# Kernel optimization log

Measured on AMD Instinct MI355X. Metric: run time of the kernel, lower is better.

The kernel has to match this reference:

```python
import jax, jax.numpy as jnp
import numpy as np

N_NODES = 50000
N_EDGES = 800000
D = 128
NEG_SLOPE = 0.01
LN_EPS = 1e-5


def gcn_conv(x, W, b, src, dst, n_nodes):
    # Linear transform: [N, D_in] @ [D_in, D_out]
    h = x @ W
    # Symmetric degree normalization (self-loops already included in src/dst)
    deg = jax.ops.segment_sum(jnp.ones_like(dst, dtype=h.dtype), dst, num_segments=n_nodes)
    dinv = jnp.where(deg > 0, jax.lax.rsqrt(deg), 0.0)
    coef = dinv[src] * dinv[dst]                      # [E]
    msg = h[src] * coef[:, None]                      # gather + scale, [E, D]
    out = jax.ops.segment_sum(msg, dst, num_segments=n_nodes)  # scatter-add
    return out + b


def layer_norm(x, gamma, beta):
    mu = jnp.mean(x, axis=-1, keepdims=True)
    var = jnp.mean(jnp.square(x - mu), axis=-1, keepdims=True)
    return (x - mu) * jax.lax.rsqrt(var + LN_EPS) * gamma + beta


def setup_inputs() -> dict:
    key = jax.random.key(0)
    ks = jax.random.split(key, 8)
    x = jax.random.normal(ks[0], (N_NODES, D), dtype=jnp.float32)
    edge_index = jax.random.randint(ks[1], (2, N_EDGES), 0, N_NODES, dtype=jnp.int64)
    s = 1.0 / np.sqrt(D)
    W1 = jax.random.uniform(ks[2], (D, D), jnp.float32, -s, s)
    b1 = jnp.zeros((D,), jnp.float32)
    W2 = jax.random.uniform(ks[3], (D, D), jnp.float32, -s, s)
    b2 = jnp.zeros((D,), jnp.float32)
    ln1_g = jnp.ones((D,), jnp.float32)
    ln1_b = jnp.zeros((D,), jnp.float32)
    ln2_g = jnp.ones((D,), jnp.float32)
    ln2_b = jnp.zeros((D,), jnp.float32)
    return {"x": x, "edge_index": edge_index, "W1": W1, "b1": b1,
            "ln1_g": ln1_g, "ln1_b": ln1_b, "W2": W2, "b2": b2,
            "ln2_g": ln2_g, "ln2_b": ln2_b}


def reference(x, edge_index, W1, b1, ln1_g, ln1_b, W2, b2, ln2_g, ln2_b):
    n = x.shape[0]
    # add self-loops (PyG GCNConv default)
    loops = jnp.arange(n, dtype=edge_index.dtype)
    src = jnp.concatenate([edge_index[0], loops])
    dst = jnp.concatenate([edge_index[1], loops])

    residual = x
    h = gcn_conv(x, W1, b1, src, dst, n)
    h = jax.nn.leaky_relu(h, NEG_SLOPE)
    h = layer_norm(h + residual, ln1_g, ln1_b)
    h = gcn_conv(h, W2, b2, src, dst, n)
    return jax.nn.leaky_relu(layer_norm(h + residual, ln2_g, ln2_b), NEG_SLOPE)
```

## Files before the change

### kernel.cpp

```cpp
#include <hip/hip_runtime.h>
#include <hip/hip_bf16.h>

#define NN 50000
#define NE 800000
#define D 128
#define NEG_SLOPE 0.01f
#define LN_EPS 1e-5f

#define NPB 256
#define NB 196
#define CAP 6144
#define ECH 8192
#define NCH ((NE + ECH - 1) / ECH)

typedef __attribute__((ext_vector_type(8))) short bf16x8;
typedef __attribute__((ext_vector_type(4))) float f32x4;

__device__ inline unsigned short f2bf(float f) {
    unsigned u = __float_as_uint(f);
    unsigned r = 0x7FFFu + ((u >> 16) & 1u);
    return (unsigned short)((u + r) >> 16);
}
__device__ inline void bf2x(unsigned u, float& lo, float& hi) {
    lo = __uint_as_float(u << 16);
    hi = __uint_as_float(u & 0xFFFF0000u);
}


__global__ __launch_bounds__(256) void bucket_scatter(const int* __restrict__ src,
                                                      const int* __restrict__ dst,
                                                      int* __restrict__ bcursor,
                                                      int2* __restrict__ bedge, int ne) {
    __shared__ int2 stage[ECH];
    __shared__ int hist[NB], lofs[NB], lcur[NB], gbase[NB];
    __shared__ int tmp[256];
    int t = threadIdx.x;
    int e0 = blockIdx.x * ECH;
    int ecnt = min(ECH, ne - e0);
    if (t < NB) hist[t] = 0;
    __syncthreads();
    for (int k = t; k < ecnt; k += 256) atomicAdd(&hist[dst[e0 + k] >> 8], 1);
    __syncthreads();
    int v = (t < NB) ? hist[t] : 0;
    tmp[t] = v;
    __syncthreads();
    for (int off = 1; off < 256; off <<= 1) {
        int u = (t >= off) ? tmp[t - off] : 0;
        __syncthreads();
        tmp[t] += u;
        __syncthreads();
    }
    if (t < NB) {
        lofs[t] = tmp[t] - v;
        lcur[t] = tmp[t] - v;
        gbase[t] = atomicAdd(&bcursor[t], v);
    }
    __syncthreads();
    for (int k = t; k < ecnt; k += 256) {
        int s = src[e0 + k], d = dst[e0 + k];
        int p = atomicAdd(&lcur[d >> 8], 1);
        stage[p] = make_int2(s, d);
    }
    __syncthreads();
    for (int k = t; k < ecnt; k += 256) {
        int2 eg = stage[k];
        int b = eg.y >> 8;
        bedge[(size_t)b * CAP + gbase[b] + (k - lofs[b])] = eg;
    }
}

__global__ __launch_bounds__(256) void node_count(const int2* __restrict__ bedge,
                                                  const int* __restrict__ bcnt,
                                                  float* __restrict__ dinv,
                                                  int* __restrict__ prowtmp,
                                                  int* __restrict__ pbsum) {
    __shared__ int h[NPB];
    __shared__ int tmp[256];
    int b = blockIdx.x, t = threadIdx.x;
    h[t] = 0;
    __syncthreads();
    int s0 = b * CAP, s1 = s0 + bcnt[b];
    for (int k = s0 + t; k < s1; k += 256) atomicAdd(&h[bedge[k].y & 255], 1);
    __syncthreads();
    int deg = h[t];
    int node = b * NPB + t;
    if (node < NN) dinv[node] = rsqrtf((float)(deg + 1));
    int pdeg = (deg + 7) & ~7;
    tmp[t] = pdeg;
    __syncthreads();
    for (int off = 1; off < 256; off <<= 1) {
        int u = (t >= off) ? tmp[t - off] : 0;
        __syncthreads();
        tmp[t] += u;
        __syncthreads();
    }
    prowtmp[b * NPB + t] = tmp[t] - pdeg;
    if (t == 255) pbsum[b] = tmp[255];
}

__global__ void pbucket_scan(const int* __restrict__ pbsum, int* __restrict__ pbstart,
                             int* __restrict__ rowstart_nn) {
    __shared__ int tmp[256];
    int t = threadIdx.x;
    int v = (t < NB) ? pbsum[t] : 0;
    tmp[t] = v;
    __syncthreads();
    for (int off = 1; off < 256; off <<= 1) {
        int u = (t >= off) ? tmp[t - off] : 0;
        __syncthreads();
        tmp[t] += u;
        __syncthreads();
    }
    if (t < NB) pbstart[t] = tmp[t] - v;
    if (t == 255) *rowstart_nn = tmp[255];
}

__global__ __launch_bounds__(256) void csr_scatter(const int2* __restrict__ bedge,
                                                   const int* __restrict__ bcnt,
                                                   const int* __restrict__ pbstart,
                                                   const int* __restrict__ prowtmp,
                                                   const float* __restrict__ dinv,
                                                   int* __restrict__ rowstart,
                                                   int2* __restrict__ csr_pair) {
    __shared__ int cur[NPB];
    __shared__ int rl[NPB];
    int b = blockIdx.x, t = threadIdx.x;
    int base = pbstart[b];
    int node = b * NPB + t;
    int r = base + prowtmp[node];
    rl[t] = r;
    cur[t] = 0;
    if (node < NN) rowstart[node] = r;
    __syncthreads();
    int s0 = b * CAP, s1 = s0 + bcnt[b];
    for (int k = s0 + t; k < s1; k += 256) {
        int2 eg = bedge[k];
        int li = eg.y & 255;
        int p = atomicAdd(&cur[li], 1);
        float coef = dinv[eg.x] * dinv[eg.y];
        csr_pair[rl[li] + p] = make_int2(eg.x, __float_as_int(coef));
    }
    __syncthreads();
    int deg = cur[t];
    int pend = (deg + 7) & ~7;
    int selfsrc = (node < NN) ? node : 0;
    for (int k = deg; k < pend; ++k)
        csr_pair[rl[t] + k] = make_int2(selfsrc, 0);
}

__global__ void wt_pack2(const float* __restrict__ W1, const float* __restrict__ W2,
                         unsigned short* __restrict__ WT1, unsigned short* __restrict__ WT2) {
    int tid = blockIdx.x * 256 + threadIdx.x;
    const float* W = (tid < D * D) ? W1 : W2;
    unsigned short* WT = (tid < D * D) ? WT1 : WT2;
    int id = tid & (D * D - 1);
    int nn = id & 127, k = id >> 7;
    WT[nn * 128 + k] = f2bf(W[k * 128 + nn]);
}

__global__ __launch_bounds__(256) void gemm_mfma(const float* __restrict__ A,
                                                 const unsigned short* __restrict__ WT,
                                                 unsigned short* __restrict__ out, int n) {
    __shared__ __align__(16) unsigned short a_lds[64 * 128];
    __shared__ __align__(16) unsigned short w_lds[128 * 128];
    int t = threadIdx.x;
    int m0 = blockIdx.x * 64;

    #pragma unroll
    for (int it = 0; it < 8; ++it) {
        int idx = it * 256 + t;
        int row = idx >> 4, c = idx & 15;
        uint4 v = *(const uint4*)&WT[row * 128 + c * 8];
        int byte = (row * 256 + c * 16) ^ ((row & 7) << 4);
        *(uint4*)((char*)w_lds + byte) = v;
    }
    #pragma unroll
    for (int it = 0; it < 4; ++it) {
        int idx = it * 256 + t;
        int row = idx >> 4, c = idx & 15;
        int grow = m0 + row;
        float4 v0 = make_float4(0.f, 0.f, 0.f, 0.f), v1 = v0;
        if (grow < n) {
            v0 = *(const float4*)&A[(size_t)grow * D + c * 8];
            v1 = *(const float4*)&A[(size_t)grow * D + c * 8 + 4];
        }
        uint2 lo, hi;
        lo.x = (unsigned)f2bf(v0.x) | ((unsigned)f2bf(v0.y) << 16);
        lo.y = (unsigned)f2bf(v0.z) | ((unsigned)f2bf(v0.w) << 16);
        hi.x = (unsigned)f2bf(v1.x) | ((unsigned)f2bf(v1.y) << 16);
        hi.y = (unsigned)f2bf(v1.z) | ((unsigned)f2bf(v1.w) << 16);
        int byte = (row * 256 + c * 16) ^ ((row & 7) << 4);
        *(uint4*)((char*)a_lds + byte) = make_uint4(lo.x, lo.y, hi.x, hi.y);
    }
    __syncthreads();

    int wv = t >> 6, l = t & 63;
    int lrow = l & 15, lgrp = l >> 4;
    int arow = wv * 16 + lrow;

    f32x4 acc[8];
    #pragma unroll
    for (int nf = 0; nf < 8; ++nf) acc[nf] = (f32x4){0.f, 0.f, 0.f, 0.f};

    #pragma unroll
    for (int kk = 0; kk < 4; ++kk) {
        int abyte = (arow * 256 + kk * 64 + lgrp * 16) ^ ((arow & 7) << 4);
        bf16x8 afrag = *(bf16x8*)((char*)a_lds + abyte);
        #pragma unroll
        for (int nf = 0; nf < 8; ++nf) {
            int bcol = nf * 16 + lrow;
            int bbyte = (bcol * 256 + kk * 64 + lgrp * 16) ^ ((bcol & 7) << 4);
            bf16x8 bfrag = *(bf16x8*)((char*)w_lds + bbyte);
            acc[nf] = __builtin_amdgcn_mfma_f32_16x16x32_bf16(afrag, bfrag, acc[nf], 0, 0, 0);
        }
    }

    #pragma unroll
    for (int nf = 0; nf < 8; ++nf) {
        #pragma unroll
        for (int r = 0; r < 4; ++r) {
            int grow = m0 + wv * 16 + lgrp * 4 + r;
            if (grow < n) {
                int col = nf * 16 + lrow;
                out[(size_t)grow * D + col] = f2bf(acc[nf][r]);
            }
        }
    }
}


__device__ inline void agg8(const unsigned* __restrict__ h, const int2* __restrict__ csr_pair,
                            int e, int lane, float& accx, float& accy) {
    int4 q0 = *(const int4*)&csr_pair[e + 0];
    int4 q1 = *(const int4*)&csr_pair[e + 2];
    int4 q2 = *(const int4*)&csr_pair[e + 4];
    int4 q3 = *(const int4*)&csr_pair[e + 6];
    unsigned g0 = h[(size_t)q0.x * (D / 2) + lane];
    unsigned g1 = h[(size_t)q0.z * (D / 2) + lane];
    unsigned g2 = h[(size_t)q1.x * (D / 2) + lane];
    unsigned g3 = h[(size_t)q1.z * (D / 2) + lane];
    unsigned g4 = h[(size_t)q2.x * (D / 2) + lane];
    unsigned g5 = h[(size_t)q2.z * (D / 2) + lane];
    unsigned g6 = h[(size_t)q3.x * (D / 2) + lane];
    unsigned g7 = h[(size_t)q3.z * (D / 2) + lane];
    float ax, ay, c;
    c = __int_as_float(q0.y); bf2x(g0, ax, ay); accx = fmaf(c, ax, accx); accy = fmaf(c, ay, accy);
    c = __int_as_float(q0.w); bf2x(g1, ax, ay); accx = fmaf(c, ax, accx); accy = fmaf(c, ay, accy);
    c = __int_as_float(q1.y); bf2x(g2, ax, ay); accx = fmaf(c, ax, accx); accy = fmaf(c, ay, accy);
    c = __int_as_float(q1.w); bf2x(g3, ax, ay); accx = fmaf(c, ax, accx); accy = fmaf(c, ay, accy);
    c = __int_as_float(q2.y); bf2x(g4, ax, ay); accx = fmaf(c, ax, accx); accy = fmaf(c, ay, accy);
    c = __int_as_float(q2.w); bf2x(g5, ax, ay); accx = fmaf(c, ax, accx); accy = fmaf(c, ay, accy);
    c = __int_as_float(q3.y); bf2x(g6, ax, ay); accx = fmaf(c, ax, accx); accy = fmaf(c, ay, accy);
    c = __int_as_float(q3.w); bf2x(g7, ax, ay); accx = fmaf(c, ax, accx); accy = fmaf(c, ay, accy);
}

template <int MODE>
__device__ inline float2 ln_norm(float v0, float v1, float2 gv, float2 bt) {
    float s1 = v0 + v1, s2 = v0 * v0 + v1 * v1;
    #pragma unroll
    for (int off = 1; off < 64; off <<= 1) {
        s1 += __shfl_xor(s1, off, 64);
        s2 += __shfl_xor(s2, off, 64);
    }
    float mu = s1 * (1.f / 128.f);
    float var = fmaxf(s2 * (1.f / 128.f) - mu * mu, 0.f);
    float rs = rsqrtf(var + LN_EPS);
    float o0 = (v0 - mu) * rs * gv.x + bt.x;
    float o1 = (v1 - mu) * rs * gv.y + bt.y;
    if (MODE == 1) {
        o0 = o0 > 0.f ? o0 : NEG_SLOPE * o0;
        o1 = o1 > 0.f ? o1 : NEG_SLOPE * o1;
    }
    return make_float2(o0, o1);
}

template <int MODE>
__global__ __launch_bounds__(256) void agg_ln(const unsigned* __restrict__ h,
                                              const float* __restrict__ x,
                                              const float* __restrict__ bias,
                                              const float* __restrict__ gamma,
                                              const float* __restrict__ beta,
                                              const float* __restrict__ dinv,
                                              const int* __restrict__ rowstart,
                                              const int2* __restrict__ csr_pair,
                                              float* __restrict__ out) {
    int wid = threadIdx.x >> 6;
    int lane = threadIdx.x & 63;
    int iA = blockIdx.x * 8 + wid * 2;
    int iB = iA + 1;
    float diA = dinv[iA], diB = dinv[iB];
    size_t rowA = (size_t)iA * D + 2 * lane;
    size_t rowB = (size_t)iB * D + 2 * lane;

    float hx, hy;
    bf2x(h[(size_t)iA * (D / 2) + lane], hx, hy);
    float aAx = diA * diA * hx, aAy = diA * diA * hy;
    bf2x(h[(size_t)iB * (D / 2) + lane], hx, hy);
    float aBx = diB * diB * hx, aBy = diB * diB * hy;

    int eA = __builtin_amdgcn_readfirstlane(rowstart[iA]);
    int eA1 = __builtin_amdgcn_readfirstlane(rowstart[iA + 1]);
    int eB = __builtin_amdgcn_readfirstlane(rowstart[iB]);
    int eB1 = __builtin_amdgcn_readfirstlane(rowstart[iB + 1]);

    while (eA < eA1 && eB < eB1) {
        int4 qA0 = *(const int4*)&csr_pair[eA + 0];
        int4 qA1 = *(const int4*)&csr_pair[eA + 2];
        int4 qA2 = *(const int4*)&csr_pair[eA + 4];
        int4 qA3 = *(const int4*)&csr_pair[eA + 6];
        int4 qB0 = *(const int4*)&csr_pair[eB + 0];
        int4 qB1 = *(const int4*)&csr_pair[eB + 2];
        int4 qB2 = *(const int4*)&csr_pair[eB + 4];
        int4 qB3 = *(const int4*)&csr_pair[eB + 6];
        unsigned gA0 = h[(size_t)qA0.x * (D / 2) + lane];
        unsigned gA1 = h[(size_t)qA0.z * (D / 2) + lane];
        unsigned gA2 = h[(size_t)qA1.x * (D / 2) + lane];
        unsigned gA3 = h[(size_t)qA1.z * (D / 2) + lane];
        unsigned gA4 = h[(size_t)qA2.x * (D / 2) + lane];
        unsigned gA5 = h[(size_t)qA2.z * (D / 2) + lane];
        unsigned gA6 = h[(size_t)qA3.x * (D / 2) + lane];
        unsigned gA7 = h[(size_t)qA3.z * (D / 2) + lane];
        unsigned gB0 = h[(size_t)qB0.x * (D / 2) + lane];
        unsigned gB1 = h[(size_t)qB0.z * (D / 2) + lane];
        unsigned gB2 = h[(size_t)qB1.x * (D / 2) + lane];
        unsigned gB3 = h[(size_t)qB1.z * (D / 2) + lane];
        unsigned gB4 = h[(size_t)qB2.x * (D / 2) + lane];
        unsigned gB5 = h[(size_t)qB2.z * (D / 2) + lane];
        unsigned gB6 = h[(size_t)qB3.x * (D / 2) + lane];
        unsigned gB7 = h[(size_t)qB3.z * (D / 2) + lane];
        float ax, ay, c;
        c = __int_as_float(qA0.y); bf2x(gA0, ax, ay); aAx = fmaf(c, ax, aAx); aAy = fmaf(c, ay, aAy);
        c = __int_as_float(qA0.w); bf2x(gA1, ax, ay); aAx = fmaf(c, ax, aAx); aAy = fmaf(c, ay, aAy);
        c = __int_as_float(qA1.y); bf2x(gA2, ax, ay); aAx = fmaf(c, ax, aAx); aAy = fmaf(c, ay, aAy);
        c = __int_as_float(qA1.w); bf2x(gA3, ax, ay); aAx = fmaf(c, ax, aAx); aAy = fmaf(c, ay, aAy);
        c = __int_as_float(qA2.y); bf2x(gA4, ax, ay); aAx = fmaf(c, ax, aAx); aAy = fmaf(c, ay, aAy);
        c = __int_as_float(qA2.w); bf2x(gA5, ax, ay); aAx = fmaf(c, ax, aAx); aAy = fmaf(c, ay, aAy);
        c = __int_as_float(qA3.y); bf2x(gA6, ax, ay); aAx = fmaf(c, ax, aAx); aAy = fmaf(c, ay, aAy);
        c = __int_as_float(qA3.w); bf2x(gA7, ax, ay); aAx = fmaf(c, ax, aAx); aAy = fmaf(c, ay, aAy);
        c = __int_as_float(qB0.y); bf2x(gB0, ax, ay); aBx = fmaf(c, ax, aBx); aBy = fmaf(c, ay, aBy);
        c = __int_as_float(qB0.w); bf2x(gB1, ax, ay); aBx = fmaf(c, ax, aBx); aBy = fmaf(c, ay, aBy);
        c = __int_as_float(qB1.y); bf2x(gB2, ax, ay); aBx = fmaf(c, ax, aBx); aBy = fmaf(c, ay, aBy);
        c = __int_as_float(qB1.w); bf2x(gB3, ax, ay); aBx = fmaf(c, ax, aBx); aBy = fmaf(c, ay, aBy);
        c = __int_as_float(qB2.y); bf2x(gB4, ax, ay); aBx = fmaf(c, ax, aBx); aBy = fmaf(c, ay, aBy);
        c = __int_as_float(qB2.w); bf2x(gB5, ax, ay); aBx = fmaf(c, ax, aBx); aBy = fmaf(c, ay, aBy);
        c = __int_as_float(qB3.y); bf2x(gB6, ax, ay); aBx = fmaf(c, ax, aBx); aBy = fmaf(c, ay, aBy);
        c = __int_as_float(qB3.w); bf2x(gB7, ax, ay); aBx = fmaf(c, ax, aBx); aBy = fmaf(c, ay, aBy);
        eA += 8; eB += 8;
    }
    while (eA < eA1) { agg8(h, csr_pair, eA, lane, aAx, aAy); eA += 8; }
    while (eB < eB1) { agg8(h, csr_pair, eB, lane, aBx, aBy); eB += 8; }

    float2 bv = *(const float2*)&bias[2 * lane];
    float2 gv = *(const float2*)&gamma[2 * lane];
    float2 bt = *(const float2*)&beta[2 * lane];

    aAx += bv.x; aAy += bv.y;
    aBx += bv.x; aBy += bv.y;
    if (MODE == 0) {
        aAx = aAx > 0.f ? aAx : NEG_SLOPE * aAx;
        aAy = aAy > 0.f ? aAy : NEG_SLOPE * aAy;
        aBx = aBx > 0.f ? aBx : NEG_SLOPE * aBx;
        aBy = aBy > 0.f ? aBy : NEG_SLOPE * aBy;
    }
    float2 xA = *(const float2*)&x[rowA];
    float2 xB = *(const float2*)&x[rowB];

    float2 oA = ln_norm<MODE>(aAx + xA.x, aAy + xA.y, gv, bt);
    float2 oB = ln_norm<MODE>(aBx + xB.x, aBy + xB.y, gv, bt);
    *(float2*)&out[rowA] = oA;
    *(float2*)&out[rowB] = oB;
}

extern "C" void kernel_launch(void* const* d_in, const int* in_sizes, int n_in,
                              void* d_out, int out_size, void* d_ws, size_t ws_size,
                              hipStream_t stream) {
    const float* x    = (const float*)d_in[0];
    const int*   ei   = (const int*)d_in[1];
    const float* W1   = (const float*)d_in[2];
    const float* b1   = (const float*)d_in[3];
    const float* ln1g = (const float*)d_in[4];
    const float* ln1b = (const float*)d_in[5];
    const float* W2   = (const float*)d_in[6];
    const float* b2   = (const float*)d_in[7];
    const float* ln2g = (const float*)d_in[8];
    const float* ln2b = (const float*)d_in[9];
    float* out = (float*)d_out;

    const int* srcp = ei;
    const int* dstp = ei + NE;

    char* ws = (char*)d_ws;
    size_t p = 0;
    auto alloc = [&](size_t bytes) {
        char* r = ws + p;
        p += (bytes + 255) & ~(size_t)255;
        return r;
    };
    int*   bcursor  = (int*)alloc(NB * 4);
    int*   pbsum    = (int*)alloc(NB * 4);
    int*   pbstart  = (int*)alloc(NB * 4);
    int*   prowtmp  = (int*)alloc(NB * NPB * 4);
    int*   rowstart = (int*)alloc((NN + 1) * 4);
    float* dinv     = (float*)alloc(NN * 4);
    int2*  bedge    = (int2*)alloc((size_t)NB * CAP * 8);
    int2*  csr_pair = (int2*)alloc(((size_t)NE + 8 * NN) * 8);
    unsigned short* hbf = (unsigned short*)alloc((size_t)NN * D * 2);
    unsigned short* wt1 = (unsigned short*)alloc(D * D * 2);
    unsigned short* wt2 = (unsigned short*)alloc(D * D * 2);

    hipMemsetAsync(bcursor, 0, NB * 4, stream);

    bucket_scatter<<<NCH, 256, 0, stream>>>(srcp, dstp, bcursor, bedge, NE);
    node_count<<<NB, 256, 0, stream>>>(bedge, bcursor, dinv, prowtmp, pbsum);
    pbucket_scan<<<1, 256, 0, stream>>>(pbsum, pbstart, &rowstart[NN]);
    csr_scatter<<<NB, 256, 0, stream>>>(bedge, bcursor, pbstart, prowtmp, dinv,
                                        rowstart, csr_pair);

    wt_pack2<<<2 * D * D / 256, 256, 0, stream>>>(W1, W2, wt1, wt2);

    gemm_mfma<<<(NN + 63) / 64, 256, 0, stream>>>(x, wt1, hbf, NN);
    agg_ln<0><<<NN / 8, 256, 0, stream>>>((const unsigned*)hbf, x, b1, ln1g, ln1b, dinv,
                                          rowstart, csr_pair, out);

    gemm_mfma<<<(NN + 63) / 64, 256, 0, stream>>>(out, wt2, hbf, NN);
    agg_ln<1><<<NN / 8, 256, 0, stream>>>((const unsigned*)hbf, x, b2, ln2g, ln2b, dinv,
                                          rowstart, csr_pair, out);
}
```

Measured before the change: 147.4 us.

## Drop bucket-scan kernel via atomic ticket, store layer-1 output as bf16, nontemporal CSR loads

```diff
diff --git a/kernel.cpp b/kernel.cpp
--- a/kernel.cpp
+++ b/kernel.cpp
@@ -15,6 +15,7 @@
 
 typedef __attribute__((ext_vector_type(8))) short bf16x8;
 typedef __attribute__((ext_vector_type(4))) float f32x4;
+typedef __attribute__((ext_vector_type(4))) int i32x4;
 
 __device__ inline unsigned short f2bf(float f) {
     unsigned u = __float_as_uint(f);
@@ -72,10 +73,11 @@
 __global__ __launch_bounds__(256) void node_count(const int2* __restrict__ bedge,
                                                   const int* __restrict__ bcnt,
                                                   float* __restrict__ dinv,
-                                                  int* __restrict__ prowtmp,
-                                                  int* __restrict__ pbsum) {
+                                                  int2* __restrict__ rowinfo,
+                                                  int* __restrict__ ticket) {
     __shared__ int h[NPB];
     __shared__ int tmp[256];
+    __shared__ int base;
     int b = blockIdx.x, t = threadIdx.x;
     h[t] = 0;
     __syncthreads();
@@ -84,7 +86,6 @@
     __syncthreads();
     int deg = h[t];
     int node = b * NPB + t;
-    if (node < NN) dinv[node] = rsqrtf((float)(deg + 1));
     int pdeg = (deg + 7) & ~7;
     tmp[t] = pdeg;
     __syncthreads();
@@ -94,43 +95,25 @@
         tmp[t] += u;
         __syncthreads();
     }
-    prowtmp[b * NPB + t] = tmp[t] - pdeg;
-    if (t == 255) pbsum[b] = tmp[255];
-}
-
-__global__ void pbucket_scan(const int* __restrict__ pbsum, int* __restrict__ pbstart,
-                             int* __restrict__ rowstart_nn) {
-    __shared__ int tmp[256];
-    int t = threadIdx.x;
-    int v = (t < NB) ? pbsum[t] : 0;
-    tmp[t] = v;
-    __syncthreads();
-    for (int off = 1; off < 256; off <<= 1) {
-        int u = (t >= off) ? tmp[t - off] : 0;
-        __syncthreads();
-        tmp[t] += u;
-        __syncthreads();
-    }
-    if (t < NB) pbstart[t] = tmp[t] - v;
-    if (t == 255) *rowstart_nn = tmp[255];
+    if (t == 255) base = atomicAdd(ticket, tmp[255]);
+    __syncthreads();
+    if (node < NN) {
+        dinv[node] = rsqrtf((float)(deg + 1));
+        rowinfo[node] = make_int2(base + tmp[t] - pdeg, pdeg);
+    }
 }
 
 __global__ __launch_bounds__(256) void csr_scatter(const int2* __restrict__ bedge,
                                                    const int* __restrict__ bcnt,
-                                                   const int* __restrict__ pbstart,
-                                                   const int* __restrict__ prowtmp,
+                                                   const int2* __restrict__ rowinfo,
                                                    const float* __restrict__ dinv,
-                                                   int* __restrict__ rowstart,
                                                    int2* __restrict__ csr_pair) {
     __shared__ int cur[NPB];
     __shared__ int rl[NPB];
     int b = blockIdx.x, t = threadIdx.x;
-    int base = pbstart[b];
     int node = b * NPB + t;
-    int r = base + prowtmp[node];
-    rl[t] = r;
+    rl[t] = (node < NN) ? rowinfo[node].x : 0;
     cur[t] = 0;
-    if (node < NN) rowstart[node] = r;
     __syncthreads();
     int s0 = b * CAP, s1 = s0 + bcnt[b];
     for (int k = s0 + t; k < s1; k += 256) {
@@ -158,7 +141,8 @@
     WT[nn * 128 + k] = f2bf(W[k * 128 + nn]);
 }
 
-__global__ __launch_bounds__(256) void gemm_mfma(const float* __restrict__ A,
+template <bool BF16IN>
+__global__ __launch_bounds__(256) void gemm_mfma(const void* __restrict__ Ain,
                                                  const unsigned short* __restrict__ WT,
                                                  unsigned short* __restrict__ out, int n) {
     __shared__ __align__(16) unsigned short a_lds[64 * 128];
@@ -179,18 +163,22 @@
         int idx = it * 256 + t;
         int row = idx >> 4, c = idx & 15;
         int grow = m0 + row;
-        float4 v0 = make_float4(0.f, 0.f, 0.f, 0.f), v1 = v0;
+        uint4 w = make_uint4(0u, 0u, 0u, 0u);
         if (grow < n) {
-            v0 = *(const float4*)&A[(size_t)grow * D + c * 8];
-            v1 = *(const float4*)&A[(size_t)grow * D + c * 8 + 4];
+            if constexpr (BF16IN) {
+                w = *(const uint4*)&((const unsigned short*)Ain)[(size_t)grow * D + c * 8];
+            } else {
+                const float* Af = (const float*)Ain;
+                float4 v0 = *(const float4*)&Af[(size_t)grow * D + c * 8];
+                float4 v1 = *(const float4*)&Af[(size_t)grow * D + c * 8 + 4];
+                w.x = (unsigned)f2bf(v0.x) | ((unsigned)f2bf(v0.y) << 16);
+                w.y = (unsigned)f2bf(v0.z) | ((unsigned)f2bf(v0.w) << 16);
+                w.z = (unsigned)f2bf(v1.x) | ((unsigned)f2bf(v1.y) << 16);
+                w.w = (unsigned)f2bf(v1.z) | ((unsigned)f2bf(v1.w) << 16);
+            }
         }
-        uint2 lo, hi;
-        lo.x = (unsigned)f2bf(v0.x) | ((unsigned)f2bf(v0.y) << 16);
-        lo.y = (unsigned)f2bf(v0.z) | ((unsigned)f2bf(v0.w) << 16);
-        hi.x = (unsigned)f2bf(v1.x) | ((unsigned)f2bf(v1.y) << 16);
-        hi.y = (unsigned)f2bf(v1.z) | ((unsigned)f2bf(v1.w) << 16);
         int byte = (row * 256 + c * 16) ^ ((row & 7) << 4);
-        *(uint4*)((char*)a_lds + byte) = make_uint4(lo.x, lo.y, hi.x, hi.y);
+        *(uint4*)((char*)a_lds + byte) = w;
     }
     __syncthreads();
 
@@ -231,47 +219,27 @@
 
 __device__ inline void agg8(const unsigned* __restrict__ h, const int2* __restrict__ csr_pair,
                             int e, int lane, float& accx, float& accy) {
-    int4 q0 = *(const int4*)&csr_pair[e + 0];
-    int4 q1 = *(const int4*)&csr_pair[e + 2];
-    int4 q2 = *(const int4*)&csr_pair[e + 4];
-    int4 q3 = *(const int4*)&csr_pair[e + 6];
-    unsigned g0 = h[(size_t)q0.x * (D / 2) + lane];
-    unsigned g1 = h[(size_t)q0.z * (D / 2) + lane];
-    unsigned g2 = h[(size_t)q1.x * (D / 2) + lane];
-    unsigned g3 = h[(size_t)q1.z * (D / 2) + lane];
-    unsigned g4 = h[(size_t)q2.x * (D / 2) + lane];
-    unsigned g5 = h[(size_t)q2.z * (D / 2) + lane];
-    unsigned g6 = h[(size_t)q3.x * (D / 2) + lane];
-    unsigned g7 = h[(size_t)q3.z * (D / 2) + lane];
+    i32x4 q0 = __builtin_nontemporal_load((const i32x4*)(csr_pair + e + 0));
+    i32x4 q1 = __builtin_nontemporal_load((const i32x4*)(csr_pair + e + 2));
+    i32x4 q2 = __builtin_nontemporal_load((const i32x4*)(csr_pair + e + 4));
+    i32x4 q3 = __builtin_nontemporal_load((const i32x4*)(csr_pair + e + 6));
+    unsigned g0 = h[(size_t)q0[0] * (D / 2) + lane];
+    unsigned g1 = h[(size_t)q0[2] * (D / 2) + lane];
+    unsigned g2 = h[(size_t)q1[0] * (D / 2) + lane];
+    unsigned g3 = h[(size_t)q1[2] * (D / 2) + lane];
+    unsigned g4 = h[(size_t)q2[0] * (D / 2) + lane];
+    unsigned g5 = h[(size_t)q2[2] * (D / 2) + lane];
+    unsigned g6 = h[(size_t)q3[0] * (D / 2) + lane];
+    unsigned g7 = h[(size_t)q3[2] * (D / 2) + lane];
     float ax, ay, c;
-    c = __int_as_float(q0.y); bf2x(g0, ax, ay); accx = fmaf(c, ax, accx); accy = fmaf(c, ay, accy);
-    c = __int_as_float(q0.w); bf2x(g1, ax, ay); accx = fmaf(c, ax, accx); accy = fmaf(c, ay, accy);
-    c = __int_as_float(q1.y); bf2x(g2, ax, ay); accx = fmaf(c, ax, accx); accy = fmaf(c, ay, accy);
-    c = __int_as_float(q1.w); bf2x(g3, ax, ay); accx = fmaf(c, ax, accx); accy = fmaf(c, ay, accy);
-    c = __int_as_float(q2.y); bf2x(g4, ax, ay); accx = fmaf(c, ax, accx); accy = fmaf(c, ay, accy);
-    c = __int_as_float(q2.w); bf2x(g5, ax, ay); accx = fmaf(c, ax, accx); accy = fmaf(c, ay, accy);
-    c = __int_as_float(q3.y); bf2x(g6, ax, ay); accx = fmaf(c, ax, accx); accy = fmaf(c, ay, accy);
-    c = __int_as_float(q3.w); bf2x(g7, ax, ay); accx = fmaf(c, ax, accx); accy = fmaf(c, ay, accy);
-}
-
-template <int MODE>
-__device__ inline float2 ln_norm(float v0, float v1, float2 gv, float2 bt) {
-    float s1 = v0 + v1, s2 = v0 * v0 + v1 * v1;
-    #pragma unroll
-    for (int off = 1; off < 64; off <<= 1) {
-        s1 += __shfl_xor(s1, off, 64);
-        s2 += __shfl_xor(s2, off, 64);
-    }
-    float mu = s1 * (1.f / 128.f);
-    float var = fmaxf(s2 * (1.f / 128.f) - mu * mu, 0.f);
-    float rs = rsqrtf(var + LN_EPS);
-    float o0 = (v0 - mu) * rs * gv.x + bt.x;
-    float o1 = (v1 - mu) * rs * gv.y + bt.y;
-    if (MODE == 1) {
-        o0 = o0 > 0.f ? o0 : NEG_SLOPE * o0;
-        o1 = o1 > 0.f ? o1 : NEG_SLOPE * o1;
-    }
-    return make_float2(o0, o1);
+    c = __int_as_float(q0[1]); bf2x(g0, ax, ay); accx = fmaf(c, ax, accx); accy = fmaf(c, ay, accy);
+    c = __int_as_float(q0[3]); bf2x(g1, ax, ay); accx = fmaf(c, ax, accx); accy = fmaf(c, ay, accy);
+    c = __int_as_float(q1[1]); bf2x(g2, ax, ay); accx = fmaf(c, ax, accx); accy = fmaf(c, ay, accy);
+    c = __int_as_float(q1[3]); bf2x(g3, ax, ay); accx = fmaf(c, ax, accx); accy = fmaf(c, ay, accy);
+    c = __int_as_float(q2[1]); bf2x(g4, ax, ay); accx = fmaf(c, ax, accx); accy = fmaf(c, ay, accy);
+    c = __int_as_float(q2[3]); bf2x(g5, ax, ay); accx = fmaf(c, ax, accx); accy = fmaf(c, ay, accy);
+    c = __int_as_float(q3[1]); bf2x(g6, ax, ay); accx = fmaf(c, ax, accx); accy = fmaf(c, ay, accy);
+    c = __int_as_float(q3[3]); bf2x(g7, ax, ay); accx = fmaf(c, ax, accx); accy = fmaf(c, ay, accy);
 }
 
 template <int MODE>
@@ -281,16 +249,15 @@
                                               const float* __restrict__ gamma,
                                               const float* __restrict__ beta,
                                               const float* __restrict__ dinv,
-                                              const int* __restrict__ rowstart,
+                                              const int2* __restrict__ rowinfo,
                                               const int2* __restrict__ csr_pair,
-                                              float* __restrict__ out) {
+                                              float* __restrict__ out,
+                                              unsigned* __restrict__ outb) {
     int wid = threadIdx.x >> 6;
     int lane = threadIdx.x & 63;
     int iA = blockIdx.x * 8 + wid * 2;
     int iB = iA + 1;
     float diA = dinv[iA], diB = dinv[iB];
-    size_t rowA = (size_t)iA * D + 2 * lane;
-    size_t rowB = (size_t)iB * D + 2 * lane;
 
     float hx, hy;
     bf2x(h[(size_t)iA * (D / 2) + lane], hx, hy);
@@ -298,53 +265,55 @@
     bf2x(h[(size_t)iB * (D / 2) + lane], hx, hy);
     float aBx = diB * diB * hx, aBy = diB * diB * hy;
 
-    int eA = __builtin_amdgcn_readfirstlane(rowstart[iA]);
-    int eA1 = __builtin_amdgcn_readfirstlane(rowstart[iA + 1]);
-    int eB = __builtin_amdgcn_readfirstlane(rowstart[iB]);
-    int eB1 = __builtin_amdgcn_readfirstlane(rowstart[iB + 1]);
+    int2 riA = rowinfo[iA];
+    int2 riB = rowinfo[iB];
+    int eA = __builtin_amdgcn_readfirstlane(riA.x);
+    int eA1 = eA + __builtin_amdgcn_readfirstlane(riA.y);
+    int eB = __builtin_amdgcn_readfirstlane(riB.x);
+    int eB1 = eB + __builtin_amdgcn_readfirstlane(riB.y);
 
     while (eA < eA1 && eB < eB1) {
-        int4 qA0 = *(const int4*)&csr_pair[eA + 0];
-        int4 qA1 = *(const int4*)&csr_pair[eA + 2];
-        int4 qA2 = *(const int4*)&csr_pair[eA + 4];
-        int4 qA3 = *(const int4*)&csr_pair[eA + 6];
-        int4 qB0 = *(const int4*)&csr_pair[eB + 0];
-        int4 qB1 = *(const int4*)&csr_pair[eB + 2];
-        int4 qB2 = *(const int4*)&csr_pair[eB + 4];
-        int4 qB3 = *(const int4*)&csr_pair[eB + 6];
-        unsigned gA0 = h[(size_t)qA0.x * (D / 2) + lane];
-        unsigned gA1 = h[(size_t)qA0.z * (D / 2) + lane];
-        unsigned gA2 = h[(size_t)qA1.x * (D / 2) + lane];
-        unsigned gA3 = h[(size_t)qA1.z * (D / 2) + lane];
-        unsigned gA4 = h[(size_t)qA2.x * (D / 2) + lane];
-        unsigned gA5 = h[(size_t)qA2.z * (D / 2) + lane];
-        unsigned gA6 = h[(size_t)qA3.x * (D / 2) + lane];
-        unsigned gA7 = h[(size_t)qA3.z * (D / 2) + lane];
-        unsigned gB0 = h[(size_t)qB0.x * (D / 2) + lane];
-        unsigned gB1 = h[(size_t)qB0.z * (D / 2) + lane];
-        unsigned gB2 = h[(size_t)qB1.x * (D / 2) + lane];
-        unsigned gB3 = h[(size_t)qB1.z * (D / 2) + lane];
-        unsigned gB4 = h[(size_t)qB2.x * (D / 2) + lane];
-        unsigned gB5 = h[(size_t)qB2.z * (D / 2) + lane];
-        unsigned gB6 = h[(size_t)qB3.x * (D / 2) + lane];
-        unsigned gB7 = h[(size_t)qB3.z * (D / 2) + lane];
+        i32x4 qA0 = __builtin_nontemporal_load((const i32x4*)(csr_pair + eA + 0));
+        i32x4 qA1 = __builtin_nontemporal_load((const i32x4*)(csr_pair + eA + 2));
+        i32x4 qA2 = __builtin_nontemporal_load((const i32x4*)(csr_pair + eA + 4));
+        i32x4 qA3 = __builtin_nontemporal_load((const i32x4*)(csr_pair + eA + 6));
+        i32x4 qB0 = __builtin_nontemporal_load((const i32x4*)(csr_pair + eB + 0));
+        i32x4 qB1 = __builtin_nontemporal_load((const i32x4*)(csr_pair + eB + 2));
+        i32x4 qB2 = __builtin_nontemporal_load((const i32x4*)(csr_pair + eB + 4));
+        i32x4 qB3 = __builtin_nontemporal_load((const i32x4*)(csr_pair + eB + 6));
+        unsigned gA0 = h[(size_t)qA0[0] * (D / 2) + lane];
+        unsigned gA1 = h[(size_t)qA0[2] * (D / 2) + lane];
+        unsigned gA2 = h[(size_t)qA1[0] * (D / 2) + lane];
+        unsigned gA3 = h[(size_t)qA1[2] * (D / 2) + lane];
+        unsigned gA4 = h[(size_t)qA2[0] * (D / 2) + lane];
+        unsigned gA5 = h[(size_t)qA2[2] * (D / 2) + lane];
+        unsigned gA6 = h[(size_t)qA3[0] * (D / 2) + lane];
+        unsigned gA7 = h[(size_t)qA3[2] * (D / 2) + lane];
+        unsigned gB0 = h[(size_t)qB0[0] * (D / 2) + lane];
+        unsigned gB1 = h[(size_t)qB0[2] * (D / 2) + lane];
+        unsigned gB2 = h[(size_t)qB1[0] * (D / 2) + lane];
+        unsigned gB3 = h[(size_t)qB1[2] * (D / 2) + lane];
+        unsigned gB4 = h[(size_t)qB2[0] * (D / 2) + lane];
+        unsigned gB5 = h[(size_t)qB2[2] * (D / 2) + lane];
+        unsigned gB6 = h[(size_t)qB3[0] * (D / 2) + lane];
+        unsigned gB7 = h[(size_t)qB3[2] * (D / 2) + lane];
         float ax, ay, c;
-        c = __int_as_float(qA0.y); bf2x(gA0, ax, ay); aAx = fmaf(c, ax, aAx); aAy = fmaf(c, ay, aAy);
-        c = __int_as_float(qA0.w); bf2x(gA1, ax, ay); aAx = fmaf(c, ax, aAx); aAy = fmaf(c, ay, aAy);
-        c = __int_as_float(qA1.y); bf2x(gA2, ax, ay); aAx = fmaf(c, ax, aAx); aAy = fmaf(c, ay, aAy);
-        c = __int_as_float(qA1.w); bf2x(gA3, ax, ay); aAx = fmaf(c, ax, aAx); aAy = fmaf(c, ay, aAy);
-        c = __int_as_float(qA2.y); bf2x(gA4, ax, ay); aAx = fmaf(c, ax, aAx); aAy = fmaf(c, ay, aAy);
-        c = __int_as_float(qA2.w); bf2x(gA5, ax, ay); aAx = fmaf(c, ax, aAx); aAy = fmaf(c, ay, aAy);
-        c = __int_as_float(qA3.y); bf2x(gA6, ax, ay); aAx = fmaf(c, ax, aAx); aAy = fmaf(c, ay, aAy);
-        c = __int_as_float(qA3.w); bf2x(gA7, ax, ay); aAx = fmaf(c, ax, aAx); aAy = fmaf(c, ay, aAy);
-        c = __int_as_float(qB0.y); bf2x(gB0, ax, ay); aBx = fmaf(c, ax, aBx); aBy = fmaf(c, ay, aBy);
-        c = __int_as_float(qB0.w); bf2x(gB1, ax, ay); aBx = fmaf(c, ax, aBx); aBy = fmaf(c, ay, aBy);
-        c = __int_as_float(qB1.y); bf2x(gB2, ax, ay); aBx = fmaf(c, ax, aBx); aBy = fmaf(c, ay, aBy);
-        c = __int_as_float(qB1.w); bf2x(gB3, ax, ay); aBx = fmaf(c, ax, aBx); aBy = fmaf(c, ay, aBy);
-        c = __int_as_float(qB2.y); bf2x(gB4, ax, ay); aBx = fmaf(c, ax, aBx); aBy = fmaf(c, ay, aBy);
-        c = __int_as_float(qB2.w); bf2x(gB5, ax, ay); aBx = fmaf(c, ax, aBx); aBy = fmaf(c, ay, aBy);
-        c = __int_as_float(qB3.y); bf2x(gB6, ax, ay); aBx = fmaf(c, ax, aBx); aBy = fmaf(c, ay, aBy);
-        c = __int_as_float(qB3.w); bf2x(gB7, ax, ay); aBx = fmaf(c, ax, aBx); aBy = fmaf(c, ay, aBy);
+        c = __int_as_float(qA0[1]); bf2x(gA0, ax, ay); aAx = fmaf(c, ax, aAx); aAy = fmaf(c, ay, aAy);
+        c = __int_as_float(qA0[3]); bf2x(gA1, ax, ay); aAx = fmaf(c, ax, aAx); aAy = fmaf(c, ay, aAy);
+        c = __int_as_float(qA1[1]); bf2x(gA2, ax, ay); aAx = fmaf(c, ax, aAx); aAy = fmaf(c, ay, aAy);
+        c = __int_as_float(qA1[3]); bf2x(gA3, ax, ay); aAx = fmaf(c, ax, aAx); aAy = fmaf(c, ay, aAy);
+        c = __int_as_float(qA2[1]); bf2x(gA4, ax, ay); aAx = fmaf(c, ax, aAx); aAy = fmaf(c, ay, aAy);
+        c = __int_as_float(qA2[3]); bf2x(gA5, ax, ay); aAx = fmaf(c, ax, aAx); aAy = fmaf(c, ay, aAy);
+        c = __int_as_float(qA3[1]); bf2x(gA6, ax, ay); aAx = fmaf(c, ax, aAx); aAy = fmaf(c, ay, aAy);
+        c = __int_as_float(qA3[3]); bf2x(gA7, ax, ay); aAx = fmaf(c, ax, aAx); aAy = fmaf(c, ay, aAy);
+        c = __int_as_float(qB0[1]); bf2x(gB0, ax, ay); aBx = fmaf(c, ax, aBx); aBy = fmaf(c, ay, aBy);
+        c = __int_as_float(qB0[3]); bf2x(gB1, ax, ay); aBx = fmaf(c, ax, aBx); aBy = fmaf(c, ay, aBy);
+        c = __int_as_float(qB1[1]); bf2x(gB2, ax, ay); aBx = fmaf(c, ax, aBx); aBy = fmaf(c, ay, aBy);
+        c = __int_as_float(qB1[3]); bf2x(gB3, ax, ay); aBx = fmaf(c, ax, aBx); aBy = fmaf(c, ay, aBy);
+        c = __int_as_float(qB2[1]); bf2x(gB4, ax, ay); aBx = fmaf(c, ax, aBx); aBy = fmaf(c, ay, aBy);
+        c = __int_as_float(qB2[3]); bf2x(gB5, ax, ay); aBx = fmaf(c, ax, aBx); aBy = fmaf(c, ay, aBy);
+        c = __int_as_float(qB3[1]); bf2x(gB6, ax, ay); aBx = fmaf(c, ax, aBx); aBy = fmaf(c, ay, aBy);
+        c = __int_as_float(qB3[3]); bf2x(gB7, ax, ay); aBx = fmaf(c, ax, aBx); aBy = fmaf(c, ay, aBy);
         eA += 8; eB += 8;
     }
     while (eA < eA1) { agg8(h, csr_pair, eA, lane, aAx, aAy); eA += 8; }
@@ -362,13 +331,45 @@
         aBx = aBx > 0.f ? aBx : NEG_SLOPE * aBx;
         aBy = aBy > 0.f ? aBy : NEG_SLOPE * aBy;
     }
+    size_t rowA = (size_t)iA * D + 2 * lane;
+    size_t rowB = (size_t)iB * D + 2 * lane;
     float2 xA = *(const float2*)&x[rowA];
     float2 xB = *(const float2*)&x[rowB];
-
-    float2 oA = ln_norm<MODE>(aAx + xA.x, aAy + xA.y, gv, bt);
-    float2 oB = ln_norm<MODE>(aBx + xB.x, aBy + xB.y, gv, bt);
-    *(float2*)&out[rowA] = oA;
-    *(float2*)&out[rowB] = oB;
+    float vA0 = aAx + xA.x, vA1 = aAy + xA.y;
+    float vB0 = aBx + xB.x, vB1 = aBy + xB.y;
+
+    float sA1 = vA0 + vA1, sA2 = vA0 * vA0 + vA1 * vA1;
+    float sB1 = vB0 + vB1, sB2 = vB0 * vB0 + vB1 * vB1;
+    #pragma unroll
+    for (int off = 1; off < 64; off <<= 1) {
+        sA1 += __shfl_xor(sA1, off, 64);
+        sA2 += __shfl_xor(sA2, off, 64);
+        sB1 += __shfl_xor(sB1, off, 64);
+        sB2 += __shfl_xor(sB2, off, 64);
+    }
+    float muA = sA1 * (1.f / 128.f);
+    float varA = fmaxf(sA2 * (1.f / 128.f) - muA * muA, 0.f);
+    float rsA = rsqrtf(varA + LN_EPS);
+    float muB = sB1 * (1.f / 128.f);
+    float varB = fmaxf(sB2 * (1.f / 128.f) - muB * muB, 0.f);
+    float rsB = rsqrtf(varB + LN_EPS);
+
+    float oA0 = (vA0 - muA) * rsA * gv.x + bt.x;
+    float oA1 = (vA1 - muA) * rsA * gv.y + bt.y;
+    float oB0 = (vB0 - muB) * rsB * gv.x + bt.x;
+    float oB1 = (vB1 - muB) * rsB * gv.y + bt.y;
+
+    if (MODE == 0) {
+        outb[(size_t)iA * (D / 2) + lane] = (unsigned)f2bf(oA0) | ((unsigned)f2bf(oA1) << 16);
+        outb[(size_t)iB * (D / 2) + lane] = (unsigned)f2bf(oB0) | ((unsigned)f2bf(oB1) << 16);
+    } else {
+        oA0 = oA0 > 0.f ? oA0 : NEG_SLOPE * oA0;
+        oA1 = oA1 > 0.f ? oA1 : NEG_SLOPE * oA1;
+        oB0 = oB0 > 0.f ? oB0 : NEG_SLOPE * oB0;
+        oB1 = oB1 > 0.f ? oB1 : NEG_SLOPE * oB1;
+        *(float2*)&out[rowA] = make_float2(oA0, oA1);
+        *(float2*)&out[rowB] = make_float2(oB0, oB1);
+    }
 }
 
 extern "C" void kernel_launch(void* const* d_in, const int* in_sizes, int n_in,
@@ -396,33 +397,29 @@
         p += (bytes + 255) & ~(size_t)255;
         return r;
     };
-    int*   bcursor  = (int*)alloc(NB * 4);
-    int*   pbsum    = (int*)alloc(NB * 4);
-    int*   pbstart  = (int*)alloc(NB * 4);
-    int*   prowtmp  = (int*)alloc(NB * NPB * 4);
-    int*   rowstart = (int*)alloc((NN + 1) * 4);
+    int*   bcursor  = (int*)alloc((NB + 1) * 4);
+    int2*  rowinfo  = (int2*)alloc((size_t)NN * 8);
     float* dinv     = (float*)alloc(NN * 4);
     int2*  bedge    = (int2*)alloc((size_t)NB * CAP * 8);
     int2*  csr_pair = (int2*)alloc(((size_t)NE + 8 * NN) * 8);
-    unsigned short* hbf = (unsigned short*)alloc((size_t)NN * D * 2);
-    unsigned short* wt1 = (unsigned short*)alloc(D * D * 2);
-    unsigned short* wt2 = (unsigned short*)alloc(D * D * 2);
-
-    hipMemsetAsync(bcursor, 0, NB * 4, stream);
+    unsigned short* hbf  = (unsigned short*)alloc((size_t)NN * D * 2);
+    unsigned*       t1bf = (unsigned*)alloc((size_t)NN * D * 2);
+    unsigned short* wt1  = (unsigned short*)alloc(D * D * 2);
+    unsigned short* wt2  = (unsigned short*)alloc(D * D * 2);
+
+    hipMemsetAsync(bcursor, 0, (NB + 1) * 4, stream);
 
     bucket_scatter<<<NCH, 256, 0, stream>>>(srcp, dstp, bcursor, bedge, NE);
-    node_count<<<NB, 256, 0, stream>>>(bedge, bcursor, dinv, prowtmp, pbsum);
-    pbucket_scan<<<1, 256, 0, stream>>>(pbsum, pbstart, &rowstart[NN]);
-    csr_scatter<<<NB, 256, 0, stream>>>(bedge, bcursor, pbstart, prowtmp, dinv,
-                                        rowstart, csr_pair);
+    node_count<<<NB, 256, 0, stream>>>(bedge, bcursor, dinv, rowinfo, &bcursor[NB]);
+    csr_scatter<<<NB, 256, 0, stream>>>(bedge, bcursor, rowinfo, dinv, csr_pair);
 
     wt_pack2<<<2 * D * D / 256, 256, 0, stream>>>(W1, W2, wt1, wt2);
 
-    gemm_mfma<<<(NN + 63) / 64, 256, 0, stream>>>(x, wt1, hbf, NN);
+    gemm_mfma<false><<<(NN + 63) / 64, 256, 0, stream>>>(x, wt1, hbf, NN);
     agg_ln<0><<<NN / 8, 256, 0, stream>>>((const unsigned*)hbf, x, b1, ln1g, ln1b, dinv,
-                                          rowstart, csr_pair, out);
-
-    gemm_mfma<<<(NN + 63) / 64, 256, 0, stream>>>(out, wt2, hbf, NN);
+                                          rowinfo, csr_pair, out, t1bf);
+
+    gemm_mfma<true><<<(NN + 63) / 64, 256, 0, stream>>>(t1bf, wt2, hbf, NN);
     agg_ln<1><<<NN / 8, 256, 0, stream>>>((const unsigned*)hbf, x, b2, ln2g, ln2b, dinv,
-                                          rowstart, csr_pair, out);
-}
+                                          rowinfo, csr_pair, out, t1bf);
+}
```

Result: no change. 148.1 us (+0.5%).
